# Kernel optimization log

Measured on AMD Instinct MI355X. Metric: run time of the kernel, lower is better.

Reference implementation:

```python
import jax, jax.numpy as jnp
import numpy as np

B = 8192          # batch
IN = 4096         # in_features
OUT = 4096        # out_features
BS = 64           # block_size
NBR = OUT // BS   # block rows = 64
NBC = IN // BS    # block cols = 64
BPR = 16


def setup_inputs() -> dict:
    key = jax.random.key(0)
    k1, k2, k3 = jax.random.split(key, 3)
    x = jax.random.normal(k1, (B, IN), dtype=jnp.float32)
    values = jax.random.normal(k2, (NBR * BPR, BS, BS), dtype=jnp.float32) * 0.02
    bias = jax.random.normal(k3, (OUT,), dtype=jnp.float32) * 0.02
    # static BSR pattern: per block-row, BPR sorted unique block-column indices
    rng = np.random.default_rng(0)
    cols = np.stack([np.sort(rng.choice(NBC, BPR, replace=False)) for _ in range(NBR)])
    col_indices = jnp.asarray(cols.reshape(-1), dtype=jnp.int32)  # [NBR*BPR]
    return {"x": x, "values": values, "bias": bias, "col_indices": col_indices}


def reference(x, values, bias, col_indices):
    # y = (A_bsr @ x.T).T + bias  ==  x @ A.T + bias, with A in BSR layout.
    xb = x.reshape(B, NBC, BS)                       # [B, nbc, bs] block columns of x
    cols = col_indices.reshape(NBR, BPR)             # [nbr, j]
    xg = xb[:, cols, :]                              # [B, nbr, j, bs] gathered input blocks
    vals = values.reshape(NBR, BPR, BS, BS)          # [nbr, j, bs_out, bs_in]
    out = jnp.einsum('rjob,Brjb->Bro', vals, xg)     # block-sparse GEMM
    return out.reshape(B, OUT) + bias
```

## Files before the change

kernel.cpp:

```cpp
#include <hip/hip_runtime.h>
#include <hip/hip_bf16.h>
#include <stdint.h>

#define B_DIM   8192
#define IN_DIM  4096
#define OUT_DIM 4096
#define BSZ     64
#define NBR_    64
#define BPR_    16
#define KTOT    1024
#define MT      256
#define BKK     32
#define NSTEP   (KTOT / BKK)

typedef __attribute__((ext_vector_type(4))) float  floatx4;
typedef __attribute__((ext_vector_type(8))) short  shortx8;
typedef __attribute__((ext_vector_type(4))) float  fragc;

static __device__ __forceinline__ unsigned short f2bf(float f) {
  __bf16 b = (__bf16)f;
  return __builtin_bit_cast(unsigned short, b);
}

__device__ __forceinline__ void gload_lds16(const void* g, void* l) {
  __builtin_amdgcn_global_load_lds(
      (const __attribute__((address_space(1))) unsigned int*)g,
      (__attribute__((address_space(3))) unsigned int*)l, 16, 0, 0);
}

__global__ __launch_bounds__(256)
void cvt2_kernel(const float* __restrict__ x, const float* __restrict__ v,
                 unsigned short* __restrict__ xb, unsigned short* __restrict__ vb,
                 int xn8, int tn8) {
  const int stride = gridDim.x * blockDim.x;
  for (int i = blockIdx.x * blockDim.x + threadIdx.x; i < tn8; i += stride) {
    const float* src; unsigned short* dst; int idx;
    if (i < xn8) { src = x; dst = xb; idx = i; }
    else         { src = v; dst = vb; idx = i - xn8; }
    floatx4 a = __builtin_nontemporal_load(((const floatx4*)src) + 2 * idx);
    floatx4 b = __builtin_nontemporal_load(((const floatx4*)src) + 2 * idx + 1);
    uint4 o;
    o.x = (unsigned int)f2bf(a.x) | ((unsigned int)f2bf(a.y) << 16);
    o.y = (unsigned int)f2bf(a.z) | ((unsigned int)f2bf(a.w) << 16);
    o.z = (unsigned int)f2bf(b.x) | ((unsigned int)f2bf(b.y) << 16);
    o.w = (unsigned int)f2bf(b.z) | ((unsigned int)f2bf(b.w) << 16);
    ((uint4*)dst)[idx] = o;
  }
}

__global__ __launch_bounds__(256, 4)
void bsr_gemm(const unsigned short* __restrict__ xb,
              const unsigned short* __restrict__ vb,
              const float* __restrict__ bias, const int* __restrict__ colidx,
              float* __restrict__ out) {
  const int r  = blockIdx.x;
  const int m0 = blockIdx.y * MT;
  const int tid  = threadIdx.x;
  const int wave = tid >> 6;
  const int lane = tid & 63;
  const int l16  = lane & 15;
  const int quad = lane >> 4;
  const int sub  = lane >> 2;
  const int slot = lane & 3;
  const int gsw  = slot ^ ((sub >> 1) & 3);
  const int csw  = quad ^ ((l16 >> 1) & 3);

  __shared__ __align__(16) unsigned short As0[MT * BKK];
  __shared__ __align__(16) unsigned short As1[MT * BKK];
  __shared__ __align__(16) unsigned short Bs0[BSZ * BKK];
  __shared__ __align__(16) unsigned short Bs1[BSZ * BKK];

  int cidx[BPR_];
  #pragma unroll
  for (int j = 0; j < BPR_; ++j)
    cidx[j] = __builtin_amdgcn_readfirstlane(colidx[r * BPR_ + j]);

  const unsigned short* gA =
      xb + (size_t)(m0 + wave * 64 + sub) * IN_DIM + gsw * 8;
  const unsigned short* gB =
      vb + ((size_t)(r * BPR_) * BSZ + wave * 16 + sub) * BSZ + gsw * 8;

  const int aoff = (wave * 64 + l16) * BKK + csw * 8;
  const int boff = l16 * BKK + csw * 8;

  fragc acc[4][4] = {};

#define STAGE(k, As, Bs)                                                      \
  {                                                                           \
    const int jb_ = (k) >> 1, kb0_ = ((k) & 1) * BKK;                         \
    const int colo_ = cidx[jb_] * BSZ + kb0_;                                 \
    _Pragma("unroll")                                                         \
    for (int i_ = 0; i_ < 4; ++i_)                                            \
      gload_lds16(gA + (size_t)i_ * 16 * IN_DIM + colo_,                      \
                  &As[(wave * 64 + i_ * 16) * BKK]);                          \
    gload_lds16(gB + (size_t)jb_ * BSZ * BSZ + kb0_,                          \
                &Bs[(wave * 16) * BKK]);                                      \
  }

#define COMP(As, Bs)                                                          \
  {                                                                           \
    shortx8 af_[4], bf_[4];                                                   \
    _Pragma("unroll")                                                         \
    for (int mi = 0; mi < 4; ++mi)                                            \
      af_[mi] = *(const shortx8*)&As[aoff + mi * 16 * BKK];                   \
    _Pragma("unroll")                                                         \
    for (int ni = 0; ni < 4; ++ni)                                            \
      bf_[ni] = *(const shortx8*)&Bs[boff + ni * 16 * BKK];                   \
    _Pragma("unroll")                                                         \
    for (int mi = 0; mi < 4; ++mi) {                                          \
      _Pragma("unroll")                                                       \
      for (int ni = 0; ni < 4; ++ni)                                          \
        acc[mi][ni] = __builtin_amdgcn_mfma_f32_16x16x32_bf16(                \
            af_[mi], bf_[ni], acc[mi][ni], 0, 0, 0);                          \
    }                                                                         \
  }

#define SYNC()                                                                \
  asm volatile("s_waitcnt vmcnt(0)" ::: "memory");                            \
  __builtin_amdgcn_s_barrier();                                               \
  asm volatile("" ::: "memory");

  STAGE(0, As0, Bs0);
  #pragma unroll
  for (int k = 0; k < NSTEP; k += 2) {
    SYNC();
    STAGE(k + 1, As1, Bs1);
    COMP(As0, Bs0);
    SYNC();
    if (k + 2 < NSTEP) STAGE(k + 2, As0, Bs0);
    COMP(As1, Bs1);
  }
#undef STAGE
#undef COMP
#undef SYNC

  #pragma unroll
  for (int ni = 0; ni < 4; ++ni) {
    const int col = r * BSZ + ni * 16 + l16;
    const float bv = bias[col];
    #pragma unroll
    for (int mi = 0; mi < 4; ++mi) {
      #pragma unroll
      for (int reg = 0; reg < 4; ++reg) {
        const int row = m0 + wave * 64 + mi * 16 + quad * 4 + reg;
        out[(size_t)row * OUT_DIM + col] = acc[mi][ni][reg] + bv;
      }
    }
  }
}

__global__ __launch_bounds__(256)
void bsr_naive(const float* __restrict__ x, const float* __restrict__ v,
               const float* __restrict__ bias, const int* __restrict__ colidx,
               float* __restrict__ out) {
  const size_t gid = (size_t)blockIdx.x * blockDim.x + threadIdx.x;
  if (gid >= (size_t)B_DIM * OUT_DIM) return;
  const int b = gid / OUT_DIM;
  const int oc = gid % OUT_DIM;
  const int rr = oc / BSZ, o = oc % BSZ;
  float s = bias[oc];
  for (int j = 0; j < BPR_; ++j) {
    const int c = colidx[rr * BPR_ + j];
    const float* xp = x + (size_t)b * IN_DIM + c * BSZ;
    const float* vp = v + ((size_t)(rr * BPR_ + j) * BSZ + o) * BSZ;
    for (int k = 0; k < BSZ; ++k) s += vp[k] * xp[k];
  }
  out[gid] = s;
}

extern "C" void kernel_launch(void* const* d_in, const int* in_sizes, int n_in,
                              void* d_out, int out_size, void* d_ws, size_t ws_size,
                              hipStream_t stream) {
  const float* x    = (const float*)d_in[0];
  const float* vals = (const float*)d_in[1];
  const float* bias = (const float*)d_in[2];
  const int*   cols = (const int*)d_in[3];
  float* out = (float*)d_out;

  const size_t x_elems = (size_t)B_DIM * IN_DIM;
  const size_t v_elems = (size_t)NBR_ * BPR_ * BSZ * BSZ;
  const size_t xb_bytes = x_elems * sizeof(unsigned short);
  const size_t vb_bytes = v_elems * sizeof(unsigned short);

  if (ws_size >= xb_bytes + vb_bytes) {
    unsigned short* xbp = (unsigned short*)d_ws;
    unsigned short* vbp = (unsigned short*)((char*)d_ws + xb_bytes);
    const int xn8 = (int)(x_elems / 8);
    const int tn8 = (int)((x_elems + v_elems) / 8);
    cvt2_kernel<<<dim3(9216), dim3(256), 0, stream>>>(x, vals, xbp, vbp, xn8, tn8);
    dim3 grid(NBR_, B_DIM / MT);
    bsr_gemm<<<grid, dim3(256), 0, stream>>>(xbp, vbp, bias, cols, out);
  } else {
    const size_t n = (size_t)B_DIM * OUT_DIM;
    bsr_naive<<<dim3((unsigned)((n + 255) / 256)), dim3(256), 0, stream>>>(
        x, vals, bias, cols, out);
  }
}
```

Baseline: 399.0 us.

## Deepen GEMM pipeline to four LDS stages and remap blocks for XCD locality

The BSR GEMM moves from double to quad buffering in shared memory, keeping three stages of global-to-LDS loads in flight and using partial vmcnt waits instead of draining all loads each step. It also flattens the grid to 1D and remaps block IDs so each XCD handles a contiguous tile of block-rows and batch rows, aiming for better L2 reuse of x and weights. The extra LDS (about 80KB) lowers the occupancy target from 4 to 2 blocks per CU, trading parallelism for latency hiding.

```diff
diff --git a/kernel.cpp b/kernel.cpp
--- a/kernel.cpp
+++ b/kernel.cpp
@@ -48,27 +48,38 @@
   }
 }
 
-__global__ __launch_bounds__(256, 4)
+__global__ __launch_bounds__(256, 2)
 void bsr_gemm(const unsigned short* __restrict__ xb,
               const unsigned short* __restrict__ vb,
               const float* __restrict__ bias, const int* __restrict__ colidx,
               float* __restrict__ out) {
-  const int r  = blockIdx.x;
-  const int m0 = blockIdx.y * MT;
+  const int bid    = blockIdx.x;
+  const int xcd    = bid & 7;
+  const int slot   = bid >> 3;
+  const int within = slot & 63;
+  const int rloc   = within >> 2;
+  const int mloc   = ((slot >> 6) << 2) | (within & 3);
+  const int r      = ((xcd & 3) << 4) | rloc;
+  const int m0     = ((((xcd >> 2) << 4) | mloc)) * MT;
+
   const int tid  = threadIdx.x;
   const int wave = tid >> 6;
   const int lane = tid & 63;
   const int l16  = lane & 15;
   const int quad = lane >> 4;
   const int sub  = lane >> 2;
-  const int slot = lane & 3;
-  const int gsw  = slot ^ ((sub >> 1) & 3);
+  const int slt  = lane & 3;
+  const int gsw  = slt ^ ((sub >> 1) & 3);
   const int csw  = quad ^ ((l16 >> 1) & 3);
 
   __shared__ __align__(16) unsigned short As0[MT * BKK];
   __shared__ __align__(16) unsigned short As1[MT * BKK];
+  __shared__ __align__(16) unsigned short As2[MT * BKK];
+  __shared__ __align__(16) unsigned short As3[MT * BKK];
   __shared__ __align__(16) unsigned short Bs0[BSZ * BKK];
   __shared__ __align__(16) unsigned short Bs1[BSZ * BKK];
+  __shared__ __align__(16) unsigned short Bs2[BSZ * BKK];
+  __shared__ __align__(16) unsigned short Bs3[BSZ * BKK];
 
   int cidx[BPR_];
   #pragma unroll
@@ -115,24 +126,34 @@
     }                                                                         \
   }
 
-#define SYNC()                                                                \
-  asm volatile("s_waitcnt vmcnt(0)" ::: "memory");                            \
-  __builtin_amdgcn_s_barrier();                                               \
-  asm volatile("" ::: "memory");
+#define ITER(k, Ac, Bc, An, Bn)                                              \
+  do {                                                                       \
+    if ((k) < NSTEP - 2)                                                     \
+      asm volatile("s_waitcnt vmcnt(10)" ::: "memory");                      \
+    else if ((k) == NSTEP - 2)                                               \
+      asm volatile("s_waitcnt vmcnt(5)" ::: "memory");                       \
+    else                                                                     \
+      asm volatile("s_waitcnt vmcnt(0)" ::: "memory");                       \
+    __builtin_amdgcn_s_barrier();                                            \
+    asm volatile("" ::: "memory");                                           \
+    if ((k) + 3 < NSTEP) { STAGE((k) + 3, An, Bn); }                         \
+    COMP(Ac, Bc);                                                            \
+  } while (0)
 
   STAGE(0, As0, Bs0);
+  STAGE(1, As1, Bs1);
+  STAGE(2, As2, Bs2);
+
   #pragma unroll
-  for (int k = 0; k < NSTEP; k += 2) {
-    SYNC();
-    STAGE(k + 1, As1, Bs1);
-    COMP(As0, Bs0);
-    SYNC();
-    if (k + 2 < NSTEP) STAGE(k + 2, As0, Bs0);
-    COMP(As1, Bs1);
+  for (int k = 0; k < NSTEP; k += 4) {
+    ITER(k + 0, As0, Bs0, As3, Bs3);
+    ITER(k + 1, As1, Bs1, As0, Bs0);
+    ITER(k + 2, As2, Bs2, As1, Bs1);
+    ITER(k + 3, As3, Bs3, As2, Bs2);
   }
 #undef STAGE
 #undef COMP
-#undef SYNC
+#undef ITER
 
   #pragma unroll
   for (int ni = 0; ni < 4; ++ni) {
@@ -188,8 +209,8 @@
     const int xn8 = (int)(x_elems / 8);
     const int tn8 = (int)((x_elems + v_elems) / 8);
     cvt2_kernel<<<dim3(9216), dim3(256), 0, stream>>>(x, vals, xbp, vbp, xn8, tn8);
-    dim3 grid(NBR_, B_DIM / MT);
-    bsr_gemm<<<grid, dim3(256), 0, stream>>>(xbp, vbp, bias, cols, out);
+    bsr_gemm<<<dim3(NBR_ * (B_DIM / MT)), dim3(256), 0, stream>>>(
+        xbp, vbp, bias, cols, out);
   } else {
     const size_t n = (size_t)B_DIM * OUT_DIM;
     bsr_naive<<<dim3((unsigned)((n + 255) / 256)), dim3(256), 0, stream>>>(
```

Result: faster. 342.0 us (-14.3%).
